# Performance work log

Hardware: AMD Instinct MI355X
Metric: run time of the kernel (lower is better)

Reference implementation:

```python
import jax, jax.numpy as jnp
import numpy as np

OUT_F, IN_F = 4096, 4096
GROUP = 128
NGROUPS = IN_F // GROUP  # 32


def setup_inputs() -> dict:
    key = jax.random.key(0)
    k1, k2, k3, k4 = jax.random.split(key, 4)
    x = jax.random.normal(k1, (4, 2048, IN_F), dtype=jnp.float32)
    # 4-bit codes stored as integers in [0, 16)
    compressed_weight = jax.random.randint(k2, (OUT_F, IN_F), 0, 16, dtype=jnp.int32)
    scale = jax.random.uniform(k3, (OUT_F, NGROUPS), dtype=jnp.float32)
    offset = jax.random.normal(k4, (OUT_F, NGROUPS), dtype=jnp.float32)
    return {"x": x, "compressed_weight": compressed_weight, "scale": scale, "offset": offset}


def reference(x, compressed_weight, scale, offset):
    # group-wise dequant: w[o, g, j] = code * scale[o, g] - offset[o, g]
    codes = compressed_weight.astype(scale.dtype).reshape(OUT_F, NGROUPS, GROUP)
    w = (codes * scale[..., None] - offset[..., None]).reshape(OUT_F, IN_F)
    # F.linear: x @ w.T  -> [B, S, OUT_F]
    return jnp.einsum('bsi,oi->bso', x, w.astype(x.dtype))
```

## Files before the change

kernel.cpp:

```cpp
#include <hip/hip_runtime.h>
#include <stdint.h>

#define OUT_F 4096
#define IN_F  4096
#define NGROUPS 32
#define BK 64
#define NT (IN_F / BK)

typedef __attribute__((ext_vector_type(4)))  float    f32x4;
typedef __attribute__((ext_vector_type(8)))  short    bf16x8;
typedef __attribute__((ext_vector_type(4)))  int      i32x4;
typedef __attribute__((ext_vector_type(4)))  uint32_t u32x4;

__device__ __forceinline__ ushort f2bf(float f) {
  union { float f; uint32_t u; } v; v.f = f;
  uint32_t r = v.u + 0x7FFFu + ((v.u >> 16) & 1u);
  return (ushort)(r >> 16);
}

__global__ void cvt_x_kernel(const float* __restrict__ x, ushort* __restrict__ xb, int n8) {
  int i = blockIdx.x * blockDim.x + threadIdx.x;
  if (i >= n8) return;
  const f32x4* xp = (const f32x4*)x;
  f32x4 a = xp[2 * i], b = xp[2 * i + 1];
  u32x4 o;
  o.x = (uint32_t)f2bf(a.x) | ((uint32_t)f2bf(a.y) << 16);
  o.y = (uint32_t)f2bf(a.z) | ((uint32_t)f2bf(a.w) << 16);
  o.z = (uint32_t)f2bf(b.x) | ((uint32_t)f2bf(b.y) << 16);
  o.w = (uint32_t)f2bf(b.z) | ((uint32_t)f2bf(b.w) << 16);
  ((u32x4*)xb)[i] = o;
}

__global__ void dequant_w_kernel(const int* __restrict__ cw,
                                 const float* __restrict__ sc,
                                 const float* __restrict__ of,
                                 ushort* __restrict__ wb) {
  int t = blockIdx.x * blockDim.x + threadIdx.x;
  int o  = t >> 9;
  int k0 = (t & 511) << 3;
  int g  = k0 >> 7;
  float s   = sc[o * NGROUPS + g];
  float off = of[o * NGROUPS + g];
  const i32x4* cp = (const i32x4*)(cw + (size_t)o * IN_F + k0);
  i32x4 c0 = cp[0], c1 = cp[1];
  u32x4 out;
  out.x = (uint32_t)f2bf((float)c0.x * s - off) | ((uint32_t)f2bf((float)c0.y * s - off) << 16);
  out.y = (uint32_t)f2bf((float)c0.z * s - off) | ((uint32_t)f2bf((float)c0.w * s - off) << 16);
  out.z = (uint32_t)f2bf((float)c1.x * s - off) | ((uint32_t)f2bf((float)c1.y * s - off) << 16);
  out.w = (uint32_t)f2bf((float)c1.z * s - off) | ((uint32_t)f2bf((float)c1.w * s - off) << 16);
  *(u32x4*)(wb + (size_t)o * IN_F + k0) = out;
}


#define BAR() do { asm volatile("" ::: "memory"); __builtin_amdgcn_s_barrier(); asm volatile("" ::: "memory"); } while (0)

#define GLLDS(gp, lp) __builtin_amdgcn_global_load_lds( \
  (const __attribute__((address_space(1))) uint32_t*)(const void*)(gp), \
  (__attribute__((address_space(3))) uint32_t*)(void*)(lp), 16, 0, 0)

#define STAGE_A(buf, kt) do { \
  _Pragma("unroll") for (int q_ = 0; q_ < 4; ++q_) \
    GLLDS(A + (size_t)(m0 + q_ * 64 + stRow) * IN_F + (kt) * BK + sl * 8, \
          ldsb + (buf) * 65536 + q_ * 8192 + wid * 1024); \
} while (0)

#define STAGE_B(buf, kt) do { \
  _Pragma("unroll") for (int q_ = 0; q_ < 4; ++q_) \
    GLLDS(B + (size_t)(n0 + q_ * 64 + stRow) * IN_F + (kt) * BK + sl * 8, \
          ldsb + (buf) * 65536 + 32768 + q_ * 8192 + wid * 1024); \
} while (0)

#define RD_AH(dst, i0, base, H, OFF) do { \
  _Pragma("unroll") for (int i_ = 0; i_ < 4; ++i_) \
    dst[i_][H] = *(const bf16x8*)((base) + ((i0) + i_) * 2048 + (OFF)); \
} while (0)

#define RD_BH(dst, j0, base, H, OFF) do { \
  _Pragma("unroll") for (int j_ = 0; j_ < 2; ++j_) \
    dst[j_][H] = *(const bf16x8*)((base) + ((j0) + j_) * 2048 + (OFF)); \
} while (0)

#define MFMAQ16(I0, J0, Aset, Bset) do { \
  __builtin_amdgcn_s_setprio(1); \
  _Pragma("unroll") for (int h_ = 0; h_ < 2; ++h_) \
  _Pragma("unroll") for (int i_ = 0; i_ < 4; ++i_) \
  _Pragma("unroll") for (int j_ = 0; j_ < 2; ++j_) \
    acc[(I0) + i_][(J0) + j_] = __builtin_amdgcn_mfma_f32_16x16x32_bf16(Aset[i_][h_], Bset[j_][h_], acc[(I0) + i_][(J0) + j_], 0, 0, 0); \
  __builtin_amdgcn_s_setprio(0); \
} while (0)

__global__ __launch_bounds__(512, 2) void gemm256(const ushort* __restrict__ A,
                                                  const ushort* __restrict__ B,
                                                  float* __restrict__ C, int M) {
  __shared__ ushort lds[65536];
  char* ldsb = (char*)lds;

  const int nmt = M >> 8;
  const int nwg = gridDim.x;
  int wg = blockIdx.x;
  if ((nwg & 7) == 0) wg = (wg & 7) * (nwg >> 3) + (wg >> 3);
  const int bn = wg / nmt;
  const int bm = wg % nmt;
  const int m0 = bm << 8, n0 = bn << 8;

  const int tid  = threadIdx.x;
  const int lane = tid & 63;
  const int wid  = tid >> 6;
  const int wr   = wid >> 2;
  const int wc   = wid & 3;

  const int stRow = wid * 8 + (lane >> 3);
  const int sl    = (lane & 7) ^ (lane >> 3);

  const int frow = lane & 15;
  const int g    = lane >> 4;
  const int off0 = frow * 128 + (((g    ) ^ (lane & 7)) << 4);
  const int off1 = frow * 128 + (((4 + g) ^ (lane & 7)) << 4);

  f32x4 acc[8][4] = {};
  bf16x8 Al[4][2], Ah[4][2], Bl[2][2], Bh[2][2];

  STAGE_A(0, 0); STAGE_B(0, 0);
  STAGE_A(1, 1); STAGE_B(1, 1);
  asm volatile("s_waitcnt vmcnt(8)" ::: "memory");
  BAR();

#pragma unroll 1
  for (int t = 0; t < NT; ++t) {
    const int cur = t & 1;
    const char* aC = ldsb + cur * 65536 + wr * 16384;
    const char* bC = ldsb + cur * 65536 + 32768 + wc * 8192;

    RD_AH(Al, 0, aC, 0, off0); RD_AH(Al, 0, aC, 1, off1);
    RD_BH(Bl, 0, bC, 0, off0); RD_BH(Bl, 0, bC, 1, off1);
    BAR();
    MFMAQ16(0, 0, Al, Bl);
    BAR();

    RD_BH(Bh, 2, bC, 0, off0); RD_BH(Bh, 2, bC, 1, off1);
    BAR();
    MFMAQ16(0, 2, Al, Bh);
    BAR();

    RD_AH(Ah, 4, aC, 0, off0); RD_AH(Ah, 4, aC, 1, off1);
    if (t + 2 < NT) STAGE_B(cur, t + 2);
    BAR();
    MFMAQ16(4, 2, Ah, Bh);
    BAR();

    if (t + 2 < NT) {
      STAGE_A(cur, t + 2);
      asm volatile("s_waitcnt vmcnt(8)" ::: "memory");
    } else if (t + 1 < NT) {
      asm volatile("s_waitcnt vmcnt(0)" ::: "memory");
    }
    BAR();
    MFMAQ16(4, 0, Ah, Bl);
    BAR();
  }

  const int crow0 = m0 + wr * 128 + (g << 2);
  const int ccol0 = n0 + wc * 64 + frow;
#pragma unroll
  for (int mf = 0; mf < 8; ++mf)
#pragma unroll
    for (int nf = 0; nf < 4; ++nf)
#pragma unroll
      for (int q = 0; q < 4; ++q)
        C[(size_t)(crow0 + mf * 16 + q) * OUT_F + (ccol0 + nf * 16)] = acc[mf][nf][q];
}

__global__ void naive_kernel(const float* __restrict__ x, const int* __restrict__ cw,
                             const float* __restrict__ sc, const float* __restrict__ of,
                             float* __restrict__ out, int M) {
  int idx = blockIdx.x * blockDim.x + threadIdx.x;
  if (idx >= M * OUT_F) return;
  int o = idx & (OUT_F - 1);
  int m = idx >> 12;
  const float* xr = x + (size_t)m * IN_F;
  const int*   wr = cw + (size_t)o * IN_F;
  float acc = 0.f;
  for (int gg = 0; gg < NGROUPS; ++gg) {
    float s = sc[o * NGROUPS + gg], off = of[o * NGROUPS + gg];
#pragma unroll 8
    for (int k = 0; k < 128; ++k) {
      int kk = (gg << 7) + k;
      acc += xr[kk] * ((float)wr[kk] * s - off);
    }
  }
  out[idx] = acc;
}

extern "C" void kernel_launch(void* const* d_in, const int* in_sizes, int n_in,
                              void* d_out, int out_size, void* d_ws, size_t ws_size,
                              hipStream_t stream) {
  const float* x  = (const float*)d_in[0];
  const int*   cw = (const int*)d_in[1];
  const float* sc = (const float*)d_in[2];
  const float* of = (const float*)d_in[3];
  float* out = (float*)d_out;
  const int M = in_sizes[0] / IN_F;

  const size_t xb_bytes = (size_t)M * IN_F * 2;
  const size_t wb_bytes = (size_t)OUT_F * IN_F * 2;

  if (ws_size >= xb_bytes + wb_bytes && (M % 256) == 0) {
    ushort* xb = (ushort*)d_ws;
    ushort* wb = (ushort*)((char*)d_ws + xb_bytes);

    int n8 = (M * IN_F) / 8;
    cvt_x_kernel<<<(n8 + 255) / 256, 256, 0, stream>>>(x, xb, n8);

    int nw8 = (OUT_F * IN_F) / 8;
    dequant_w_kernel<<<(nw8 + 255) / 256, 256, 0, stream>>>(cw, sc, of, wb);

    dim3 grid((M / 256) * (OUT_F / 256));
    gemm256<<<grid, 512, 0, stream>>>(xb, wb, out, M);
  } else {
    int total = M * OUT_F;
    naive_kernel<<<(total + 255) / 256, 256, 0, stream>>>(x, cw, sc, of, out, M);
  }
}
```

Measured before the change: 302.5 us.

## Restructure GEMM main loop into two-tile unrolled pipeline with finer-grained staging

The 256x256 bf16 GEMM main loop is unrolled by two K-tiles with fixed LDS buffer pointers. Global-to-LDS staging is split into half-tiles issued across more phases, and A-register sets are merged to reduce register pressure. Explicit lgkmcnt/vmcnt waits replace the coarser waits. The aim is to overlap memory traffic with MFMA better and free registers, at the risk of subtle synchronization hazards when a buffer is overwritten while still being read.

```diff
diff --git a/kernel.cpp b/kernel.cpp
--- a/kernel.cpp
+++ b/kernel.cpp
@@ -6,6 +6,7 @@
 #define NGROUPS 32
 #define BK 64
 #define NT (IN_F / BK)
+#define NITER (NT / 2)
 
 typedef __attribute__((ext_vector_type(4)))  float    f32x4;
 typedef __attribute__((ext_vector_type(8)))  short    bf16x8;
@@ -53,21 +54,25 @@
 
 
 #define BAR() do { asm volatile("" ::: "memory"); __builtin_amdgcn_s_barrier(); asm volatile("" ::: "memory"); } while (0)
+#define LGKM0() asm volatile("s_waitcnt lgkmcnt(0)" ::: "memory")
+#define LGKM8() asm volatile("s_waitcnt lgkmcnt(8)" ::: "memory")
+#define VM4()   asm volatile("s_waitcnt vmcnt(4)" ::: "memory")
+#define VM0()   asm volatile("s_waitcnt vmcnt(0)" ::: "memory")
 
 #define GLLDS(gp, lp) __builtin_amdgcn_global_load_lds( \
   (const __attribute__((address_space(1))) uint32_t*)(const void*)(gp), \
   (__attribute__((address_space(3))) uint32_t*)(void*)(lp), 16, 0, 0)
 
-#define STAGE_A(buf, kt) do { \
-  _Pragma("unroll") for (int q_ = 0; q_ < 4; ++q_) \
-    GLLDS(A + (size_t)(m0 + q_ * 64 + stRow) * IN_F + (kt) * BK + sl * 8, \
-          ldsb + (buf) * 65536 + q_ * 8192 + wid * 1024); \
-} while (0)
-
-#define STAGE_B(buf, kt) do { \
-  _Pragma("unroll") for (int q_ = 0; q_ < 4; ++q_) \
-    GLLDS(B + (size_t)(n0 + q_ * 64 + stRow) * IN_F + (kt) * BK + sl * 8, \
-          ldsb + (buf) * 65536 + 32768 + q_ * 8192 + wid * 1024); \
+#define STAGE_AH(buf, kt, h_) do { \
+  _Pragma("unroll") for (int c_ = 0; c_ < 2; ++c_) \
+    GLLDS(A + (size_t)(m0 + (h_) * 128 + c_ * 64 + stRow) * IN_F + (kt) * BK + sl * 8, \
+          ldsb + (buf) * 65536 + (h_) * 16384 + c_ * 8192 + wid * 1024); \
+} while (0)
+
+#define STAGE_BH(buf, kt, h_) do { \
+  _Pragma("unroll") for (int c_ = 0; c_ < 2; ++c_) \
+    GLLDS(B + (size_t)(n0 + (h_) * 128 + c_ * 64 + stRow) * IN_F + (kt) * BK + sl * 8, \
+          ldsb + (buf) * 65536 + 32768 + (h_) * 16384 + c_ * 8192 + wid * 1024); \
 } while (0)
 
 #define RD_AH(dst, i0, base, H, OFF) do { \
@@ -118,44 +123,72 @@
   const int off1 = frow * 128 + (((4 + g) ^ (lane & 7)) << 4);
 
   f32x4 acc[8][4] = {};
-  bf16x8 Al[4][2], Ah[4][2], Bl[2][2], Bh[2][2];
-
-  STAGE_A(0, 0); STAGE_B(0, 0);
-  STAGE_A(1, 1); STAGE_B(1, 1);
-  asm volatile("s_waitcnt vmcnt(8)" ::: "memory");
+  bf16x8 Ar[4][2], Bl[2][2], Bh[2][2];
+
+  const char* aX = ldsb + wr * 16384;
+  const char* bX = ldsb + 32768 + wc * 8192;
+  const char* aY = ldsb + 65536 + wr * 16384;
+  const char* bY = ldsb + 65536 + 32768 + wc * 8192;
+
+  STAGE_AH(0, 0, 0); STAGE_AH(0, 0, 1);
+  STAGE_BH(0, 0, 0); STAGE_BH(0, 0, 1);
+  STAGE_BH(1, 1, 0); STAGE_BH(1, 1, 1);
+  VM4();
   BAR();
 
 #pragma unroll 1
-  for (int t = 0; t < NT; ++t) {
-    const int cur = t & 1;
-    const char* aC = ldsb + cur * 65536 + wr * 16384;
-    const char* bC = ldsb + cur * 65536 + 32768 + wc * 8192;
-
-    RD_AH(Al, 0, aC, 0, off0); RD_AH(Al, 0, aC, 1, off1);
-    RD_BH(Bl, 0, bC, 0, off0); RD_BH(Bl, 0, bC, 1, off1);
-    BAR();
-    MFMAQ16(0, 0, Al, Bl);
-    BAR();
-
-    RD_BH(Bh, 2, bC, 0, off0); RD_BH(Bh, 2, bC, 1, off1);
-    BAR();
-    MFMAQ16(0, 2, Al, Bh);
-    BAR();
-
-    RD_AH(Ah, 4, aC, 0, off0); RD_AH(Ah, 4, aC, 1, off1);
-    if (t + 2 < NT) STAGE_B(cur, t + 2);
-    BAR();
-    MFMAQ16(4, 2, Ah, Bh);
-    BAR();
-
-    if (t + 2 < NT) {
-      STAGE_A(cur, t + 2);
-      asm volatile("s_waitcnt vmcnt(8)" ::: "memory");
-    } else if (t + 1 < NT) {
-      asm volatile("s_waitcnt vmcnt(0)" ::: "memory");
-    }
-    BAR();
-    MFMAQ16(4, 0, Ah, Bl);
+  for (int j = 0; j < NITER; ++j) {
+    const int tY = 2 * j + 1;
+    const bool more = (j + 1 < NITER);
+
+    RD_AH(Ar, 0, aX, 0, off0); RD_AH(Ar, 0, aX, 1, off1);
+    RD_BH(Bl, 0, bX, 0, off0); RD_BH(Bl, 0, bX, 1, off1);
+    STAGE_AH(1, tY, 0);
+    LGKM8();
+    BAR(); LGKM0();
+    MFMAQ16(0, 0, Ar, Bl);
+    BAR();
+
+    RD_BH(Bh, 2, bX, 0, off0); RD_BH(Bh, 2, bX, 1, off1);
+    STAGE_AH(1, tY, 1);
+    BAR(); LGKM0();
+    MFMAQ16(0, 2, Ar, Bh);
+    BAR();
+
+    RD_AH(Ar, 4, aX, 0, off0); RD_AH(Ar, 4, aX, 1, off1);
+    if (more) STAGE_BH(0, tY + 1, 0);
+    BAR(); LGKM0();
+    MFMAQ16(4, 2, Ar, Bh);
+    BAR();
+
+    if (more) { STAGE_BH(0, tY + 1, 1); VM4(); } else { VM0(); }
+    BAR();
+    MFMAQ16(4, 0, Ar, Bl);
+    BAR();
+
+    RD_AH(Ar, 0, aY, 0, off0); RD_AH(Ar, 0, aY, 1, off1);
+    RD_BH(Bl, 0, bY, 0, off0); RD_BH(Bl, 0, bY, 1, off1);
+    if (more) STAGE_AH(0, tY + 1, 0);
+    LGKM8();
+    BAR(); LGKM0();
+    MFMAQ16(0, 0, Ar, Bl);
+    BAR();
+
+    RD_BH(Bh, 2, bY, 0, off0); RD_BH(Bh, 2, bY, 1, off1);
+    if (more) STAGE_AH(0, tY + 1, 1);
+    BAR(); LGKM0();
+    MFMAQ16(0, 2, Ar, Bh);
+    BAR();
+
+    RD_AH(Ar, 4, aY, 0, off0); RD_AH(Ar, 4, aY, 1, off1);
+    if (more) STAGE_BH(1, tY + 2, 0);
+    BAR(); LGKM0();
+    MFMAQ16(4, 2, Ar, Bh);
+    BAR();
+
+    if (more) { STAGE_BH(1, tY + 2, 1); VM4(); }
+    BAR();
+    MFMAQ16(4, 0, Ar, Bl);
     BAR();
   }
 
@@ -204,7 +237,7 @@
   const size_t xb_bytes = (size_t)M * IN_F * 2;
   const size_t wb_bytes = (size_t)OUT_F * IN_F * 2;
 
-  if (ws_size >= xb_bytes + wb_bytes && (M % 256) == 0) {
+  if (ws_size >= xb_bytes + wb_bytes && (M % 256) == 0 && (M / 256) >= 1) {
     ushort* xb = (ushort*)d_ws;
     ushort* wb = (ushort*)((char*)d_ws + xb_bytes);
 
```

Result: faster. 289.1 us (-4.4%).

## Restructure GEMM main loop into K-half phases with ping-pong wave scheduling

Applied to the files above, without the earlier changes.

Reorganizes the bf16 GEMM inner loop to process each 64-wide K tile as two 32-wide halves with four-wide B fragments, cutting the per-iteration barriers from eight to two. Register prefetch of the next tile's fragments is overlapped with the current MFMAs. The two halves of the workgroup run differently ordered schedules so that one wave group's LDS reads line up with the other's MFMAs. The intent is to remove barrier stalls and hide LDS latency. The risks are more register pressure and subtle LDS buffer hazards across the two schedules.

```diff
diff --git a/kernel.cpp b/kernel.cpp
--- a/kernel.cpp
+++ b/kernel.cpp
@@ -53,39 +53,42 @@
 
 
 #define BAR() do { asm volatile("" ::: "memory"); __builtin_amdgcn_s_barrier(); asm volatile("" ::: "memory"); } while (0)
+#define LGKM0() asm volatile("s_waitcnt lgkmcnt(0)" ::: "memory")
+#define VM8() asm volatile("s_waitcnt vmcnt(8)" ::: "memory")
+#define VM4() asm volatile("s_waitcnt vmcnt(4)" ::: "memory")
+#define VM0() asm volatile("s_waitcnt vmcnt(0)" ::: "memory")
 
 #define GLLDS(gp, lp) __builtin_amdgcn_global_load_lds( \
   (const __attribute__((address_space(1))) uint32_t*)(const void*)(gp), \
   (__attribute__((address_space(3))) uint32_t*)(void*)(lp), 16, 0, 0)
 
-#define STAGE_A(buf, kt) do { \
-  _Pragma("unroll") for (int q_ = 0; q_ < 4; ++q_) \
-    GLLDS(A + (size_t)(m0 + q_ * 64 + stRow) * IN_F + (kt) * BK + sl * 8, \
-          ldsb + (buf) * 65536 + q_ * 8192 + wid * 1024); \
-} while (0)
-
-#define STAGE_B(buf, kt) do { \
-  _Pragma("unroll") for (int q_ = 0; q_ < 4; ++q_) \
-    GLLDS(B + (size_t)(n0 + q_ * 64 + stRow) * IN_F + (kt) * BK + sl * 8, \
-          ldsb + (buf) * 65536 + 32768 + q_ * 8192 + wid * 1024); \
-} while (0)
-
-#define RD_AH(dst, i0, base, H, OFF) do { \
+#define STAGE_AH(buf, kt, h_) do { \
+  _Pragma("unroll") for (int c_ = 0; c_ < 2; ++c_) \
+    GLLDS(A + (size_t)(m0 + (h_) * 128 + c_ * 64 + stRow) * IN_F + (kt) * BK + sl * 8, \
+          ldsb + (buf) * 65536 + (h_) * 16384 + c_ * 8192 + wid * 1024); \
+} while (0)
+
+#define STAGE_BH(buf, kt, h_) do { \
+  _Pragma("unroll") for (int c_ = 0; c_ < 2; ++c_) \
+    GLLDS(B + (size_t)(n0 + (h_) * 128 + c_ * 64 + stRow) * IN_F + (kt) * BK + sl * 8, \
+          ldsb + (buf) * 65536 + 32768 + (h_) * 16384 + c_ * 8192 + wid * 1024); \
+} while (0)
+
+#define RD_A4(dst, i0, base, OFF) do { \
   _Pragma("unroll") for (int i_ = 0; i_ < 4; ++i_) \
-    dst[i_][H] = *(const bf16x8*)((base) + ((i0) + i_) * 2048 + (OFF)); \
-} while (0)
-
-#define RD_BH(dst, j0, base, H, OFF) do { \
-  _Pragma("unroll") for (int j_ = 0; j_ < 2; ++j_) \
-    dst[j_][H] = *(const bf16x8*)((base) + ((j0) + j_) * 2048 + (OFF)); \
-} while (0)
-
-#define MFMAQ16(I0, J0, Aset, Bset) do { \
+    dst[i_] = *(const bf16x8*)((base) + ((i0) + i_) * 2048 + (OFF)); \
+} while (0)
+
+#define RD_B4(dst, base, OFF) do { \
+  _Pragma("unroll") for (int j_ = 0; j_ < 4; ++j_) \
+    dst[j_] = *(const bf16x8*)((base) + j_ * 2048 + (OFF)); \
+} while (0)
+
+#define MFMA16(I0, Aset, Bset) do { \
   __builtin_amdgcn_s_setprio(1); \
-  _Pragma("unroll") for (int h_ = 0; h_ < 2; ++h_) \
   _Pragma("unroll") for (int i_ = 0; i_ < 4; ++i_) \
-  _Pragma("unroll") for (int j_ = 0; j_ < 2; ++j_) \
-    acc[(I0) + i_][(J0) + j_] = __builtin_amdgcn_mfma_f32_16x16x32_bf16(Aset[i_][h_], Bset[j_][h_], acc[(I0) + i_][(J0) + j_], 0, 0, 0); \
+  _Pragma("unroll") for (int j_ = 0; j_ < 4; ++j_) \
+    acc[(I0) + i_][j_] = __builtin_amdgcn_mfma_f32_16x16x32_bf16(Aset[i_], Bset[j_], acc[(I0) + i_][j_], 0, 0, 0); \
   __builtin_amdgcn_s_setprio(0); \
 } while (0)
 
@@ -118,45 +121,69 @@
   const int off1 = frow * 128 + (((4 + g) ^ (lane & 7)) << 4);
 
   f32x4 acc[8][4] = {};
-  bf16x8 Al[4][2], Ah[4][2], Bl[2][2], Bh[2][2];
-
-  STAGE_A(0, 0); STAGE_B(0, 0);
-  STAGE_A(1, 1); STAGE_B(1, 1);
-  asm volatile("s_waitcnt vmcnt(8)" ::: "memory");
+  bf16x8 Aa[4], Ab[4], B0[4], B1[4];
+
+  STAGE_AH(0, 0, 0); STAGE_AH(0, 0, 1);
+  STAGE_BH(0, 0, 0); STAGE_BH(0, 0, 1);
+  STAGE_AH(1, 1, 0); STAGE_AH(1, 1, 1);
+  STAGE_BH(1, 1, 0); STAGE_BH(1, 1, 1);
+  VM8();
   BAR();
-
+  RD_A4(Aa, 0, ldsb + wr * 16384, off0);
+  RD_B4(B0, ldsb + 32768 + wc * 8192, off0);
+
+  if (wid < 4) {
 #pragma unroll 1
-  for (int t = 0; t < NT; ++t) {
-    const int cur = t & 1;
-    const char* aC = ldsb + cur * 65536 + wr * 16384;
-    const char* bC = ldsb + cur * 65536 + 32768 + wc * 8192;
-
-    RD_AH(Al, 0, aC, 0, off0); RD_AH(Al, 0, aC, 1, off1);
-    RD_BH(Bl, 0, bC, 0, off0); RD_BH(Bl, 0, bC, 1, off1);
-    BAR();
-    MFMAQ16(0, 0, Al, Bl);
-    BAR();
-
-    RD_BH(Bh, 2, bC, 0, off0); RD_BH(Bh, 2, bC, 1, off1);
-    BAR();
-    MFMAQ16(0, 2, Al, Bh);
-    BAR();
-
-    RD_AH(Ah, 4, aC, 0, off0); RD_AH(Ah, 4, aC, 1, off1);
-    if (t + 2 < NT) STAGE_B(cur, t + 2);
-    BAR();
-    MFMAQ16(4, 2, Ah, Bh);
-    BAR();
-
-    if (t + 2 < NT) {
-      STAGE_A(cur, t + 2);
-      asm volatile("s_waitcnt vmcnt(8)" ::: "memory");
-    } else if (t + 1 < NT) {
-      asm volatile("s_waitcnt vmcnt(0)" ::: "memory");
+    for (int t = 0; t < NT; ++t) {
+      const int cur = t & 1, nxt = cur ^ 1;
+      const char* aC = ldsb + cur * 65536 + wr * 16384;
+      const char* bC = ldsb + cur * 65536 + 32768 + wc * 8192;
+      const char* aN = ldsb + nxt * 65536 + wr * 16384;
+      const char* bN = ldsb + nxt * 65536 + 32768 + wc * 8192;
+
+      MFMA16(0, Aa, B0);
+      RD_A4(Ab, 4, aC, off0);
+      MFMA16(4, Ab, B0);
+      RD_A4(Aa, 0, aC, off1);
+      RD_B4(B1, bC, off1);
+      LGKM0();
+      BAR();
+      if (t + 2 < NT) { STAGE_BH(cur, t + 2, 0); STAGE_BH(cur, t + 2, 1); }
+      MFMA16(0, Aa, B1);
+      RD_A4(Ab, 4, aC, off1);
+      LGKM0();
+      if (t + 2 < NT) VM4(); else if (t + 1 < NT) VM0();
+      BAR();
+      if (t + 2 < NT) { STAGE_AH(cur, t + 2, 0); STAGE_AH(cur, t + 2, 1); }
+      MFMA16(4, Ab, B1);
+      if (t + 1 < NT) { RD_A4(Aa, 0, aN, off0); RD_B4(B0, bN, off0); }
     }
-    BAR();
-    MFMAQ16(4, 0, Ah, Bl);
-    BAR();
+  } else {
+#pragma unroll 1
+    for (int t = 0; t < NT; ++t) {
+      const int cur = t & 1, nxt = cur ^ 1;
+      const char* aC = ldsb + cur * 65536 + wr * 16384;
+      const char* bC = ldsb + cur * 65536 + 32768 + wc * 8192;
+      const char* aN = ldsb + nxt * 65536 + wr * 16384;
+      const char* bN = ldsb + nxt * 65536 + 32768 + wc * 8192;
+
+      RD_A4(Ab, 4, aC, off0);
+      MFMA16(0, Aa, B0);
+      RD_A4(Aa, 0, aC, off1);
+      RD_B4(B1, bC, off1);
+      MFMA16(4, Ab, B0);
+      LGKM0();
+      BAR();
+      if (t + 2 < NT) { STAGE_BH(cur, t + 2, 0); STAGE_BH(cur, t + 2, 1); }
+      RD_A4(Ab, 4, aC, off1);
+      MFMA16(0, Aa, B1);
+      LGKM0();
+      if (t + 2 < NT) VM4(); else if (t + 1 < NT) VM0();
+      BAR();
+      if (t + 2 < NT) { STAGE_AH(cur, t + 2, 0); STAGE_AH(cur, t + 2, 1); }
+      if (t + 1 < NT) { RD_A4(Aa, 0, aN, off0); RD_B4(B0, bN, off0); }
+      MFMA16(4, Ab, B1);
+    }
   }
 
   const int crow0 = m0 + wr * 128 + (g << 2);
```

Result: faster. 286.3 us (median of 5 runs) (-5.4%).
